# Kernel tuning notes

Measured on AMD Instinct MI355X. Metric: run time of the kernel, lower is better.

The kernel has to match this reference:

```python
import jax, jax.numpy as jnp
import numpy as np

D = 1024
D_PRE_HEAD = 128
H = 16
D_ROPE = D_PRE_HEAD // 2          # 64
DC_V = D_PRE_HEAD                 # 128
DC_KV = D_PRE_HEAD // 8           # 16
DC_Q = D // 4                     # 256
Q_HEAD_DIM = D_PRE_HEAD + D_ROPE  # 192
MEG_D = D_PRE_HEAD + DC_V         # 256
MAX_LEN = 8192
EPS = 1e-7


def rms_norm(x, w):
    x32 = x.astype(jnp.float32)
    var = jnp.mean(x32 * x32, axis=-1, keepdims=True)
    return w * (x32 * jax.lax.rsqrt(var + EPS)).astype(x.dtype)


def rope_cos_sin():
    inv_freq = 1.0 / (10000.0 ** (jnp.arange(0, D_ROPE, 2, dtype=jnp.float32) / D_ROPE))
    freqs = jnp.outer(jnp.arange(MAX_LEN, dtype=jnp.float32), inv_freq)
    emb = jnp.concatenate([freqs, freqs], axis=-1)  # [MAX_LEN, D_ROPE]
    return jnp.cos(emb), jnp.sin(emb)


def rope_reshape(x):
    # view(...,d//2,2).transpose(-1,-2).reshape == concat(even, odd) along last dim
    return jnp.concatenate([x[..., 0::2], x[..., 1::2]], axis=-1)


def rope_rotate(x):
    h = x.shape[-1] // 2
    return jnp.concatenate([-x[..., h:], x[..., :h]], axis=-1)


def setup_inputs() -> dict:
    key = jax.random.key(0)
    ks = jax.random.split(key, 12)
    B, SQ, SKV = 2, 2048, 2048
    s = 0.02
    return {
        "q_inputs": jax.random.normal(ks[0], (B, SQ, D), jnp.float32),
        "kv_input": jax.random.normal(ks[1], (B, SKV, D), jnp.float32),
        "q_pos_ids": jax.random.randint(ks[2], (B, SQ), 0, MAX_LEN),
        "kv_pos_ids": jax.random.randint(ks[3], (B, SKV), 0, MAX_LEN),
        # weights stored as [in, out] (torch Linear weight transposed)
        "Wq_down": jax.random.normal(ks[4], (D, DC_Q), jnp.float32) * s,
        "q_norm_w": jnp.ones((DC_Q,), jnp.float32),
        "Wq_up": jax.random.normal(ks[5], (DC_Q, H * Q_HEAD_DIM), jnp.float32) * s,
        "Wkv_down": jax.random.normal(ks[6], (D, DC_KV + D_ROPE), jnp.float32) * s,
        "kv_norm_w": jnp.ones((DC_KV,), jnp.float32),
        "Wkv_up": jax.random.normal(ks[7], (DC_KV, H * MEG_D), jnp.float32) * s,
        "Wout": jax.random.normal(ks[8], (H * DC_V, D), jnp.float32) * s,
    }


def reference(q_inputs, kv_input, q_pos_ids, kv_pos_ids,
              Wq_down, q_norm_w, Wq_up, Wkv_down, kv_norm_w, Wkv_up, Wout):
    B, SQ, _ = q_inputs.shape
    SKV = kv_input.shape[1]

    # query path: low-rank down -> RMSNorm -> up
    q = rms_norm(q_inputs @ Wq_down, q_norm_w) @ Wq_up
    q = q.reshape(B, SQ, H, Q_HEAD_DIM).transpose(0, 2, 1, 3)  # [B,H,SQ,192]
    q_nope, q_rope = q[..., :D_PRE_HEAD], q[..., D_PRE_HEAD:]

    # kv path: compressed latent + decoupled rope slice
    ckv_full = kv_input @ Wkv_down                              # [B,SKV,DC_KV+D_ROPE]
    c_kv, k_rope = ckv_full[..., :DC_KV], ckv_full[..., DC_KV:]
    c_kv = rms_norm(c_kv, kv_norm_w)
    kv = (c_kv @ Wkv_up).reshape(B, SKV, H, MEG_D).transpose(0, 2, 1, 3)
    k_nope, value = kv[..., :D_PRE_HEAD], kv[..., D_PRE_HEAD:]  # [B,H,SKV,128] each
    k_rope = k_rope[:, None, :, :]                              # [B,1,SKV,64]

    # RoPE with per-token position ids
    cos, sin = rope_cos_sin()
    q_cos, q_sin = cos[q_pos_ids][:, None], sin[q_pos_ids][:, None]   # [B,1,SQ,64]
    k_cos, k_sin = cos[kv_pos_ids][:, None], sin[kv_pos_ids][:, None]
    qr = rope_reshape(q_rope)
    kr = rope_reshape(k_rope)
    q_rope = qr * q_cos + rope_rotate(qr) * q_sin
    k_rope = kr * k_cos + rope_rotate(kr) * k_sin

    query = jnp.concatenate([q_nope, q_rope], axis=-1)                         # [B,H,SQ,192]
    key_t = jnp.concatenate([k_nope, jnp.broadcast_to(k_rope, (B, H, SKV, D_ROPE))], axis=-1)

    scale = 1.0 / jnp.sqrt(jnp.asarray(Q_HEAD_DIM, query.dtype))
    scores = jnp.einsum('bhqd,bhkd->bhqk', query, key_t) * scale
    attn = jax.nn.softmax(scores, axis=-1)
    out = jnp.einsum('bhqk,bhkd->bhqd', attn, value)                           # [B,H,SQ,128]
    out = out.transpose(0, 2, 1, 3).reshape(B, SQ, H * DC_V)
    return out @ Wout
```

## Files before the change

kernel.cpp:

```cpp
#include <hip/hip_runtime.h>

typedef unsigned short u16;
typedef unsigned int u32;
typedef u16 u16x4 __attribute__((ext_vector_type(4)));
typedef u16 u16x8 __attribute__((ext_vector_type(8)));
typedef u32 u32x4 __attribute__((ext_vector_type(4)));
typedef float f32x4 __attribute__((ext_vector_type(4)));
typedef __bf16 bf16x8 __attribute__((ext_vector_type(8)));
typedef __bf16 bf16x2 __attribute__((ext_vector_type(2)));

#define DEV static __device__ __forceinline__

DEV float bf2f(u16 u) { u32 v = ((u32)u) << 16; float f; __builtin_memcpy(&f, &v, 4); return f; }
DEV u16 f2bf(float f) { u32 v; __builtin_memcpy(&v, &f, 4); v += 0x7fffu + ((v >> 16) & 1u); return (u16)(v >> 16); }
DEV bf16x8 ld_frag(const u16* p) { u16x8 v = *(const u16x8*)p; return __builtin_bit_cast(bf16x8, v); }

#define LOG10000 9.210340372f

__global__ __launch_bounds__(256) void k_wtrans5(
    const float* __restrict__ Wqd, const float* __restrict__ Wqu, const float* __restrict__ Wkvd,
    const float* __restrict__ Wkvu, const float* __restrict__ Wo,
    u16* __restrict__ WqdT, u16* __restrict__ WquT, u16* __restrict__ WkvdT,
    u16* __restrict__ WkvuT, u16* __restrict__ WoT) {
  __shared__ float tile[32][33];
  int id = blockIdx.x;
  const float* in; u16* out; int R, C, Rp, bx, by;
  if (id < 256)       { in = Wqd;  out = WqdT;  R = 1024; C = 256;  Rp = 1024; bx = id & 7;  by = id >> 3; }
  else if (id < 1024) { id -= 256;  in = Wqu;  out = WquT;  R = 256;  C = 3072; Rp = 256;  bx = id % 96; by = id / 96; }
  else if (id < 1152) { id -= 1024; in = Wkvd; out = WkvdT; R = 1024; C = 80;   Rp = 1024; bx = id & 3;  by = id >> 2; }
  else if (id < 1280) { id -= 1152; in = Wkvu; out = WkvuT; R = 16;   C = 4096; Rp = 32;   bx = id;      by = 0; }
  else                { id -= 1280; in = Wo;   out = WoT;   R = 2048; C = 1024; Rp = 2048; bx = id & 31; by = id >> 5; }
  int c0 = bx * 32, r0 = by * 32;
  int tx = threadIdx.x & 31, ty = threadIdx.x >> 5;
#pragma unroll
  for (int p = 0; p < 4; p++) {
    int r = r0 + ty + p * 8, c = c0 + tx;
    tile[ty + p * 8][tx] = (r < R && c < C) ? in[(size_t)r * C + c] : 0.f;
  }
  __syncthreads();
#pragma unroll
  for (int p = 0; p < 4; p++)
    out[(size_t)(c0 + ty + p * 8) * Rp + r0 + tx] = f2bf(tile[tx][ty + p * 8]);
}

DEV void gemm64f_body(int m0, int n0, const float* __restrict__ A, const u16* __restrict__ Bt,
                      float* __restrict__ C, int N, int K, int tid, u16* As, u16* Bs) {
  constexpr int LSTR = 40;
  const int l = tid & 63, w = tid >> 6;
  const int wr = (w >> 1) * 32, wc = (w & 1) * 32;
  const int lr = l & 15, lk = (l >> 4) * 8;
  const int sr = tid >> 2, sc = (tid & 3) * 8;
  f32x4 acc[2][2] = {};
  const float* pa0 = A + (size_t)(m0 + sr) * K + sc;
  const u16* pb0 = Bt + (size_t)(n0 + sr) * K + sc;
  f32x4 vaa = *(const f32x4*)pa0, vab = *(const f32x4*)(pa0 + 4);
  u16x8 vb0 = *(const u16x8*)pb0;
  for (int k0 = 0; k0 < K; k0 += 32) {
    u16x8 va0 = { f2bf(vaa[0]), f2bf(vaa[1]), f2bf(vaa[2]), f2bf(vaa[3]),
                  f2bf(vab[0]), f2bf(vab[1]), f2bf(vab[2]), f2bf(vab[3]) };
    *(u16x8*)&As[sr * LSTR + sc] = va0;
    *(u16x8*)&Bs[sr * LSTR + sc] = vb0;
    __syncthreads();
    if (k0 + 32 < K) {
      vaa = *(const f32x4*)(pa0 + k0 + 32);
      vab = *(const f32x4*)(pa0 + k0 + 36);
      vb0 = *(const u16x8*)(pb0 + k0 + 32);
    }
    bf16x8 af[2], bf[2];
#pragma unroll
    for (int i = 0; i < 2; i++) af[i] = ld_frag(&As[(wr + i * 16 + lr) * LSTR + lk]);
#pragma unroll
    for (int j = 0; j < 2; j++) bf[j] = ld_frag(&Bs[(wc + j * 16 + lr) * LSTR + lk]);
#pragma unroll
    for (int i = 0; i < 2; i++)
#pragma unroll
      for (int j = 0; j < 2; j++)
        acc[i][j] = __builtin_amdgcn_mfma_f32_16x16x32_bf16(af[i], bf[j], acc[i][j], 0, 0, 0);
    __syncthreads();
  }
#pragma unroll
  for (int i = 0; i < 2; i++)
#pragma unroll
    for (int j = 0; j < 2; j++) {
      int row = m0 + wr + i * 16 + (l >> 4) * 4;
      int col = n0 + wc + j * 16 + lr;
#pragma unroll
      for (int r = 0; r < 4; r++)
        C[(size_t)(row + r) * N + col] = acc[i][j][r];
    }
}

__global__ __launch_bounds__(256) void k_downs(const float* __restrict__ q_in, const float* __restrict__ kv_in,
                                               const u16* __restrict__ WqdT, const u16* __restrict__ WkvdT,
                                               float* __restrict__ cq, float* __restrict__ ckvf) {
  __shared__ u16 As[64 * 40], Bs[64 * 40];
  int id = blockIdx.x, tid = threadIdx.x;
  if (id < 128) {
    int swzb = (id & 7) * 16 + (id >> 3);
    gemm64f_body((swzb >> 1) * 64, (swzb & 1) * 64, kv_in, WkvdT, ckvf, 128, 1024, tid, As, Bs);
  } else {
    int lin = id - 128;
    int swzb = (lin & 7) * 32 + (lin >> 3);
    gemm64f_body((swzb >> 2) * 64, (swzb & 3) * 64, q_in, WqdT, cq, 256, 1024, tid, As, Bs);
  }
}

__global__ __launch_bounds__(256) void k_norms(const float* __restrict__ ckvf, const float* __restrict__ kvnw,
                                               const int* __restrict__ kpos, u16* __restrict__ ckvn,
                                               u16* __restrict__ kropeb,
                                               const float* __restrict__ cq, const float* __restrict__ qnw,
                                               u16* __restrict__ cqn, float scale) {
  int id = blockIdx.x, tid = threadIdx.x;
  int l = tid & 63;
  if (id < 1024) {
    int row = id * 4 + (tid >> 6);
    const float* x = ckvf + (size_t)row * 128;
    float v = (l < 16) ? x[l] : 0.f;
    float ss = v * v;
    ss += __shfl_xor(ss, 1); ss += __shfl_xor(ss, 2); ss += __shfl_xor(ss, 4); ss += __shfl_xor(ss, 8);
    if (l < 16) ckvn[(size_t)row * 32 + l] = f2bf(v * rsqrtf(ss * (1.f / 16.f) + 1e-7f) * kvnw[l]);
    if (l >= 16 && l < 32) ckvn[(size_t)row * 32 + l] = 0;
    if (l < 32) {
      float invf = __expf(-(LOG10000 / 32.f) * (float)l);
      float ang = (float)kpos[row] * invf;
      float c = cosf(ang), s = sinf(ang);
      float e = x[16 + 2 * l], o = x[17 + 2 * l];
      kropeb[(size_t)row * 64 + l]      = f2bf(e * c - o * s);
      kropeb[(size_t)row * 64 + l + 32] = f2bf(o * c + e * s);
    }
  } else {
    int row = (id - 1024) * 4 + (tid >> 6);
    const float* x = cq + (size_t)row * 256;
    f32x4 v = *(const f32x4*)(x + l * 4);
    float ss = v[0] * v[0] + v[1] * v[1] + v[2] * v[2] + v[3] * v[3];
#pragma unroll
    for (int m = 1; m < 64; m <<= 1) ss += __shfl_xor(ss, m);
    float rinv = rsqrtf(ss * (1.f / 256.f) + 1e-7f) * scale;
    const f32x4 wv = *(const f32x4*)(qnw + l * 4);
    u16x4 o = { f2bf(v[0] * rinv * wv[0]), f2bf(v[1] * rinv * wv[1]),
                f2bf(v[2] * rinv * wv[2]), f2bf(v[3] * rinv * wv[3]) };
    *(u16x4*)(cqn + (size_t)row * 256 + l * 4) = o;
  }
}

template <int MODE>
DEV void gemm128_body(int m0, int n0, const u16* __restrict__ A, const u16* __restrict__ Bt,
                      u16* __restrict__ C0, u16* __restrict__ C1, int N, int K, int tid,
                      u16* As, u16* Bs) {
  constexpr int LSTR = 40;
  const int l = tid & 63, w = tid >> 6;
  const int wr = (w >> 1) * 64, wc = (w & 1) * 64;
  const int lr = l & 15, lk = (l >> 4) * 8;
  const int sr = tid >> 2, sc = (tid & 3) * 8;
  f32x4 acc[4][4] = {};
  const u16* pa0 = A + (size_t)(m0 + sr) * K + sc;
  const u16* pa1 = A + (size_t)(m0 + 64 + sr) * K + sc;
  const u16* pb0 = Bt + (size_t)(n0 + sr) * K + sc;
  const u16* pb1 = Bt + (size_t)(n0 + 64 + sr) * K + sc;
  u16x8 va0 = *(const u16x8*)pa0, va1 = *(const u16x8*)pa1;
  u16x8 vb0 = *(const u16x8*)pb0, vb1 = *(const u16x8*)pb1;
  for (int k0 = 0; k0 < K; k0 += 32) {
    *(u16x8*)&As[sr * LSTR + sc] = va0;
    *(u16x8*)&As[(64 + sr) * LSTR + sc] = va1;
    *(u16x8*)&Bs[sr * LSTR + sc] = vb0;
    *(u16x8*)&Bs[(64 + sr) * LSTR + sc] = vb1;
    __syncthreads();
    if (k0 + 32 < K) {
      va0 = *(const u16x8*)(pa0 + k0 + 32);
      va1 = *(const u16x8*)(pa1 + k0 + 32);
      vb0 = *(const u16x8*)(pb0 + k0 + 32);
      vb1 = *(const u16x8*)(pb1 + k0 + 32);
    }
    bf16x8 af[4], bf[4];
#pragma unroll
    for (int i = 0; i < 4; i++) af[i] = ld_frag(&As[(wr + i * 16 + lr) * LSTR + lk]);
#pragma unroll
    for (int j = 0; j < 4; j++) bf[j] = ld_frag(&Bs[(wc + j * 16 + lr) * LSTR + lk]);
#pragma unroll
    for (int i = 0; i < 4; i++)
#pragma unroll
      for (int j = 0; j < 4; j++)
        acc[i][j] = __builtin_amdgcn_mfma_f32_16x16x32_bf16(af[i], bf[j], acc[i][j], 0, 0, 0);
    __syncthreads();
  }
  if (MODE == 0 || (n0 & 255) < 128) {
#pragma unroll
    for (int i = 0; i < 4; i++)
#pragma unroll
      for (int j = 0; j < 4; j++) {
        int row = m0 + wr + i * 16 + (l >> 4) * 4;
        int col = n0 + wc + j * 16 + lr;
#pragma unroll
        for (int r = 0; r < 4; r++)
          C0[(size_t)(row + r) * N + col] = f2bf(acc[i][j][r]);
      }
  } else {
#pragma unroll
    for (int i = 0; i < 4; i++)
#pragma unroll
      for (int j = 0; j < 4; j++) {
        int row = m0 + wr + i * 16 + (l >> 4) * 4;
        int col = n0 + wc + j * 16 + lr;
        int bb = row >> 11, srow = row & 2047;
        int hh2 = col >> 8, d = col & 127;
        u16x4 pk = { f2bf(acc[i][j][0]), f2bf(acc[i][j][1]),
                     f2bf(acc[i][j][2]), f2bf(acc[i][j][3]) };
        *(u16x4*)&C1[((size_t)(bb * 16 + hh2) * 128 + d) * 2048 + srow] = pk;
      }
  }
}

__global__ __launch_bounds__(256) void k_ups(const u16* __restrict__ ckvn, const u16* __restrict__ WkvuT,
                                             u16* __restrict__ Ckv, u16* __restrict__ VTb,
                                             const u16* __restrict__ cqn, const u16* __restrict__ WquT,
                                             u16* __restrict__ qproj) {
  __shared__ u16 As[128 * 40], Bs[128 * 40];
  int id = blockIdx.x, tid = threadIdx.x;
  if (id < 1024) {
    int swzb = (id & 7) * 128 + (id >> 3);
    gemm128_body<1>((swzb >> 5) * 128, (swzb & 31) * 128, ckvn, WkvuT, Ckv, VTb, 4096, 32, tid, As, Bs);
  } else {
    int lin = id - 1024;
    int swzb = (lin & 7) * 96 + (lin >> 3);
    gemm128_body<0>((swzb / 24) * 128, (swzb % 24) * 128, cqn, WquT, qproj, nullptr, 3072, 256, tid, As, Bs);
  }
}

__global__ __launch_bounds__(256) void k_gemmh(const u16* __restrict__ A, const u16* __restrict__ Bt,
                                               float* __restrict__ Cv, int M, int N, int K) {
  constexpr int LSTR = 40;
  __shared__ u16 As[64 * LSTR], Bs[128 * LSTR];
  const int tid = threadIdx.x, l = tid & 63, w = tid >> 6;
  const int nwg = gridDim.x * gridDim.y;
  const int lin = blockIdx.y * gridDim.x + blockIdx.x;
  const int swzb = (lin & 7) * (nwg >> 3) + (lin >> 3);
  const int m0 = (swzb / gridDim.x) * 64, n0 = (swzb % gridDim.x) * 128;
  const int wr = (w >> 1) * 32, wc = (w & 1) * 64;
  const int lr = l & 15, lk = (l >> 4) * 8;
  const int sr = tid >> 2, sc = (tid & 3) * 8;
  f32x4 acc[2][4] = {};
  const u16* pa0 = A + (size_t)(m0 + sr) * K + sc;
  const u16* pb0 = Bt + (size_t)(n0 + sr) * K + sc;
  const u16* pb1 = Bt + (size_t)(n0 + 64 + sr) * K + sc;
  u16x8 va0 = *(const u16x8*)pa0;
  u16x8 vb0 = *(const u16x8*)pb0, vb1 = *(const u16x8*)pb1;
  for (int k0 = 0; k0 < K; k0 += 32) {
    *(u16x8*)&As[sr * LSTR + sc] = va0;
    *(u16x8*)&Bs[sr * LSTR + sc] = vb0;
    *(u16x8*)&Bs[(64 + sr) * LSTR + sc] = vb1;
    __syncthreads();
    if (k0 + 32 < K) {
      va0 = *(const u16x8*)(pa0 + k0 + 32);
      vb0 = *(const u16x8*)(pb0 + k0 + 32);
      vb1 = *(const u16x8*)(pb1 + k0 + 32);
    }
    bf16x8 af[2], bf[4];
#pragma unroll
    for (int i = 0; i < 2; i++) af[i] = ld_frag(&As[(wr + i * 16 + lr) * LSTR + lk]);
#pragma unroll
    for (int j = 0; j < 4; j++) bf[j] = ld_frag(&Bs[(wc + j * 16 + lr) * LSTR + lk]);
#pragma unroll
    for (int i = 0; i < 2; i++)
#pragma unroll
      for (int j = 0; j < 4; j++)
        acc[i][j] = __builtin_amdgcn_mfma_f32_16x16x32_bf16(af[i], bf[j], acc[i][j], 0, 0, 0);
    __syncthreads();
  }
#pragma unroll
  for (int i = 0; i < 2; i++)
#pragma unroll
    for (int j = 0; j < 4; j++) {
      int row = m0 + wr + i * 16 + (l >> 4) * 4;
      int col = n0 + wc + j * 16 + lr;
#pragma unroll
      for (int r = 0; r < 4; r++)
        Cv[(size_t)(row + r) * N + col] = acc[i][j][r];
    }
}

__global__ __launch_bounds__(256) void k_qrope(u16* __restrict__ q, const int* __restrict__ pos) {
  __shared__ float cs[32], sn[32];
  int bs = blockIdx.x, tid = threadIdx.x;
  if (tid < 32) {
    float invf = __expf(-(LOG10000 / 32.f) * (float)tid);
    float ang = (float)pos[bs] * invf;
    cs[tid] = cosf(ang); sn[tid] = sinf(ang);
  }
  __syncthreads();
  u16* base = q + (size_t)bs * 3072;
  int h0 = tid >> 5, p0 = tid & 31;
  int h1 = h0 + 8, p1 = p0;
  u16* r0p = base + h0 * 192 + 128;
  u16* r1p = base + h1 * 192 + 128;
  float e0 = bf2f(r0p[2 * p0]), o0 = bf2f(r0p[2 * p0 + 1]);
  float e1 = bf2f(r1p[2 * p1]), o1 = bf2f(r1p[2 * p1 + 1]);
  __syncthreads();
  r0p[p0]      = f2bf(e0 * cs[p0] - o0 * sn[p0]);
  r0p[p0 + 32] = f2bf(o0 * cs[p0] + e0 * sn[p0]);
  r1p[p1]      = f2bf(e1 * cs[p1] - o1 * sn[p1]);
  r1p[p1 + 32] = f2bf(o1 * cs[p1] + e1 * sn[p1]);
}

__global__ __launch_bounds__(512, 2) void k_attn(const u16* __restrict__ Qp, const u16* __restrict__ Ckv,
                                                 const u16* __restrict__ kropeb, const u16* __restrict__ VT,
                                                 u16* __restrict__ AO) {
  __shared__ u16 Ks[64 * 192];
  __shared__ u16 Vs[128 * 64];
  const int tid = threadIdx.x, l = tid & 63, w = tid >> 6;
  const int lr = l & 15, g = l >> 4, lk = g * 8;
  const int bid = blockIdx.x, bh = bid & 31, qt = bid >> 5;
  const int b = bh >> 4, hh = bh & 15;
  const int m0 = qt * 128;
  const u32 swz = (u32)(lr & 7) << 3;

  bf16x8 qa[6];
  {
    const u16* qrow = Qp + (size_t)(b * 2048 + m0 + w * 16 + lr) * 3072 + hh * 192;
#pragma unroll
    for (int kk = 0; kk < 6; kk++) qa[kk] = ld_frag(qrow + kk * 32 + lk);
  }

  const u16* kptr[3]; int kstep[3]; u32 klds[3];
#pragma unroll
  for (int p = 0; p < 3; p++) {
    int c2 = tid + p * 512;
    int r = c2 / 24, cc = c2 - r * 24;
    klds[p] = (u32)(r * 192 + cc * 8) ^ ((u32)(r & 7) << 3);
    if (cc < 16) { kptr[p] = Ckv + ((size_t)(b * 2048 + r)) * 4096 + hh * 256 + cc * 8; kstep[p] = 64 * 4096; }
    else         { kptr[p] = kropeb + ((size_t)(b * 2048 + r)) * 64 + (cc - 16) * 8;    kstep[p] = 64 * 64; }
  }
  const u16* vptr[2]; u32 vlds[2];
#pragma unroll
  for (int p = 0; p < 2; p++) {
    int c2 = tid + p * 512;
    int d = c2 >> 3, cc = c2 & 7;
    vlds[p] = (u32)(d * 64 + cc * 8) ^ ((u32)(d & 7) << 3);
    vptr[p] = VT + ((size_t)bh * 128 + d) * 2048 + cc * 8;
  }
  u16x8 kreg[3], vreg[2];
#pragma unroll
  for (int p = 0; p < 3; p++) { kreg[p] = *(const u16x8*)kptr[p]; kptr[p] += kstep[p]; }
#pragma unroll
  for (int p = 0; p < 2; p++) { vreg[p] = *(const u16x8*)vptr[p]; vptr[p] += 64; }

  f32x4 oacc[8] = {};
  float lsum = 0.f;
  const int srcA = lr + ((l & 16) << 1);
  const int srcB = srcA + 16;
  const bool hi = (l & 32) != 0;

  for (int t = 0; t < 32; t++) {
#pragma unroll
    for (int p = 0; p < 3; p++) *(u16x8*)&Ks[klds[p]] = kreg[p];
#pragma unroll
    for (int p = 0; p < 2; p++) *(u16x8*)&Vs[vlds[p]] = vreg[p];
    __syncthreads();
    if (t + 1 < 32) {
#pragma unroll
      for (int p = 0; p < 3; p++) { kreg[p] = *(const u16x8*)kptr[p]; kptr[p] += kstep[p]; }
#pragma unroll
      for (int p = 0; p < 2; p++) { vreg[p] = *(const u16x8*)vptr[p]; vptr[p] += 64; }
    }
    f32x4 sacc[4] = {};
    __builtin_amdgcn_s_setprio(1);
#pragma unroll
    for (int n = 0; n < 4; n++)
#pragma unroll
      for (int kk = 0; kk < 6; kk++)
        sacc[n] = __builtin_amdgcn_mfma_f32_16x16x32_bf16(
            ld_frag(&Ks[(u32)((n * 16 + lr) * 192 + kk * 32 + lk) ^ swz]), qa[kk], sacc[n], 0, 0, 0);
    __builtin_amdgcn_s_setprio(0);
    u32 pw[4][2];
#pragma unroll
    for (int n = 0; n < 4; n++) {
      float p0 = __expf(sacc[n][0]), p1 = __expf(sacc[n][1]),
            p2 = __expf(sacc[n][2]), p3 = __expf(sacc[n][3]);
      lsum += (p0 + p1) + (p2 + p3);
      bf16x2 a01 = { (__bf16)p0, (__bf16)p1 };
      bf16x2 a23 = { (__bf16)p2, (__bf16)p3 };
      pw[n][0] = __builtin_bit_cast(u32, a01);
      pw[n][1] = __builtin_bit_cast(u32, a23);
    }
    u32 pa32[2][4];
#pragma unroll
    for (int kk2 = 0; kk2 < 2; kk2++) {
      u32 t0a = __shfl(pw[2 * kk2][0], srcA), t1a = __shfl(pw[2 * kk2 + 1][0], srcA);
      u32 t0b = __shfl(pw[2 * kk2][1], srcA), t1b = __shfl(pw[2 * kk2 + 1][1], srcA);
      u32 t0c = __shfl(pw[2 * kk2][0], srcB), t1c = __shfl(pw[2 * kk2 + 1][0], srcB);
      u32 t0d = __shfl(pw[2 * kk2][1], srcB), t1d = __shfl(pw[2 * kk2 + 1][1], srcB);
      pa32[kk2][0] = hi ? t1a : t0a;
      pa32[kk2][1] = hi ? t1b : t0b;
      pa32[kk2][2] = hi ? t1c : t0c;
      pa32[kk2][3] = hi ? t1d : t0d;
    }
    __builtin_amdgcn_s_setprio(1);
#pragma unroll
    for (int kk2 = 0; kk2 < 2; kk2++) {
      u32x4 pv = { pa32[kk2][0], pa32[kk2][1], pa32[kk2][2], pa32[kk2][3] };
      bf16x8 paf = __builtin_bit_cast(bf16x8, pv);
#pragma unroll
      for (int n2 = 0; n2 < 8; n2++)
        oacc[n2] = __builtin_amdgcn_mfma_f32_16x16x32_bf16(
            paf, ld_frag(&Vs[(u32)((n2 * 16 + lr) * 64 + kk2 * 32 + lk) ^ swz]), oacc[n2], 0, 0, 0);
    }
    __builtin_amdgcn_s_setprio(0);
    __syncthreads();
  }
  float s = lsum;
  s += __shfl_xor(s, 16);
  s += __shfl_xor(s, 32);
  float rl = 1.f / s;
  float rlv[4];
#pragma unroll
  for (int r = 0; r < 4; r++) rlv[r] = __shfl(rl, g * 4 + r);
#pragma unroll
  for (int n2 = 0; n2 < 8; n2++)
#pragma unroll
    for (int r = 0; r < 4; r++) {
      int row = m0 + w * 16 + g * 4 + r;
      AO[((size_t)(b * 2048 + row) * 16 + hh) * 128 + n2 * 16 + lr] = f2bf(oacc[n2][r] * rlv[r]);
    }
}

extern "C" void kernel_launch(void* const* d_in, const int* in_sizes, int n_in,
                              void* d_out, int out_size, void* d_ws, size_t ws_size,
                              hipStream_t stream) {
  const float* q_in  = (const float*)d_in[0];
  const float* kv_in = (const float*)d_in[1];
  const int*   qpos  = (const int*)d_in[2];
  const int*   kpos  = (const int*)d_in[3];
  const float* Wqd   = (const float*)d_in[4];
  const float* qnw   = (const float*)d_in[5];
  const float* Wqu   = (const float*)d_in[6];
  const float* Wkvd  = (const float*)d_in[7];
  const float* kvnw  = (const float*)d_in[8];
  const float* Wkvu  = (const float*)d_in[9];
  const float* Wo    = (const float*)d_in[10];
  float* out = (float*)d_out;
  char* ws = (char*)d_ws;
  size_t off = 0;
  auto alloc = [&](size_t bytes) -> void* {
    void* p = ws + off; off += (bytes + 255) & ~(size_t)255; return p;
  };
  u16*   WqdT   = (u16*)alloc(256ull * 1024 * 2);
  u16*   WquT   = (u16*)alloc(3072ull * 256 * 2);
  u16*   WkvdT  = (u16*)alloc(128ull * 1024 * 2);
  u16*   WkvuT  = (u16*)alloc(4096ull * 32 * 2);
  u16*   WoT    = (u16*)alloc(1024ull * 2048 * 2);
  float* ckvf   = (float*)alloc(4096ull * 128 * 4);
  u16*   ckvn   = (u16*)alloc(4096ull * 32 * 2);
  u16*   kropeb = (u16*)alloc(4096ull * 64 * 2);
  u16*   Ckv    = (u16*)alloc(4096ull * 4096 * 2);
  u16*   VTb    = (u16*)alloc(32ull * 128 * 2048 * 2);
  float* cq     = (float*)alloc(4096ull * 256 * 4);
  u16*   cqn    = (u16*)alloc(4096ull * 256 * 2);
  u16*   qproj  = (u16*)alloc(4096ull * 3072 * 2);
  u16*   AOb    = (u16*)alloc(4096ull * 2048 * 2);
  (void)in_sizes; (void)n_in; (void)out_size; (void)ws_size;

  k_wtrans5<<<3328, 256, 0, stream>>>(Wqd, Wqu, Wkvd, Wkvu, Wo, WqdT, WquT, WkvdT, WkvuT, WoT);
  k_downs<<<384, 256, 0, stream>>>(q_in, kv_in, WqdT, WkvdT, cq, ckvf);
  k_norms<<<2048, 256, 0, stream>>>(ckvf, kvnw, kpos, ckvn, kropeb, cq, qnw, cqn, 0.07216878364870322f);
  k_ups<<<1792, 256, 0, stream>>>(ckvn, WkvuT, Ckv, VTb, cqn, WquT, qproj);
  k_qrope<<<4096, 256, 0, stream>>>(qproj, qpos);
  k_attn<<<512, 512, 0, stream>>>(qproj, Ckv, kropeb, VTb, AOb);
  k_gemmh<<<dim3(8, 64), 256, 0, stream>>>(AOb, WoT, out, 4096, 1024, 2048);
}
```

Before: 213.1 us.

## Fuse query RoPE into attention and double the KV tile to 128

Removes the standalone query-RoPE kernel. The rotation is now applied inside the attention kernel while the Q fragments are loaded into registers, with cos/sin computed per lane. This saves a kernel launch and a full read-modify-write pass over the query projection. The KV tile per iteration also grows from 64 to 128 keys, halving the loop trips and barriers. The cost is 80KB of LDS per block, which makes two blocks per CU a tight fit, plus more live registers for staging and probabilities, so spills are possible.

```diff
diff --git a/kernel.cpp b/kernel.cpp
--- a/kernel.cpp
+++ b/kernel.cpp
@@ -278,34 +278,11 @@
     }
 }
 
-__global__ __launch_bounds__(256) void k_qrope(u16* __restrict__ q, const int* __restrict__ pos) {
-  __shared__ float cs[32], sn[32];
-  int bs = blockIdx.x, tid = threadIdx.x;
-  if (tid < 32) {
-    float invf = __expf(-(LOG10000 / 32.f) * (float)tid);
-    float ang = (float)pos[bs] * invf;
-    cs[tid] = cosf(ang); sn[tid] = sinf(ang);
-  }
-  __syncthreads();
-  u16* base = q + (size_t)bs * 3072;
-  int h0 = tid >> 5, p0 = tid & 31;
-  int h1 = h0 + 8, p1 = p0;
-  u16* r0p = base + h0 * 192 + 128;
-  u16* r1p = base + h1 * 192 + 128;
-  float e0 = bf2f(r0p[2 * p0]), o0 = bf2f(r0p[2 * p0 + 1]);
-  float e1 = bf2f(r1p[2 * p1]), o1 = bf2f(r1p[2 * p1 + 1]);
-  __syncthreads();
-  r0p[p0]      = f2bf(e0 * cs[p0] - o0 * sn[p0]);
-  r0p[p0 + 32] = f2bf(o0 * cs[p0] + e0 * sn[p0]);
-  r1p[p1]      = f2bf(e1 * cs[p1] - o1 * sn[p1]);
-  r1p[p1 + 32] = f2bf(o1 * cs[p1] + e1 * sn[p1]);
-}
-
 __global__ __launch_bounds__(512, 2) void k_attn(const u16* __restrict__ Qp, const u16* __restrict__ Ckv,
                                                  const u16* __restrict__ kropeb, const u16* __restrict__ VT,
-                                                 u16* __restrict__ AO) {
-  __shared__ u16 Ks[64 * 192];
-  __shared__ u16 Vs[128 * 64];
+                                                 const int* __restrict__ qpos, u16* __restrict__ AO) {
+  __shared__ u16 Ks[128 * 192];
+  __shared__ u16 Vs[128 * 128];
   const int tid = threadIdx.x, l = tid & 63, w = tid >> 6;
   const int lr = l & 15, g = l >> 4, lk = g * 8;
   const int bid = blockIdx.x, bh = bid & 31, qt = bid >> 5;
@@ -315,33 +292,50 @@
 
   bf16x8 qa[6];
   {
-    const u16* qrow = Qp + (size_t)(b * 2048 + m0 + w * 16 + lr) * 3072 + hh * 192;
-#pragma unroll
-    for (int kk = 0; kk < 6; kk++) qa[kk] = ld_frag(qrow + kk * 32 + lk);
-  }
-
-  const u16* kptr[3]; int kstep[3]; u32 klds[3];
-#pragma unroll
-  for (int p = 0; p < 3; p++) {
+    const int rowi = b * 2048 + m0 + w * 16 + lr;
+    const u16* qrow = Qp + (size_t)rowi * 3072 + hh * 192;
+#pragma unroll
+    for (int kk = 0; kk < 4; kk++) qa[kk] = ld_frag(qrow + kk * 32 + lk);
+    u16x8 e0 = *(const u16x8*)(qrow + 128 + 16 * g);
+    u16x8 e1 = *(const u16x8*)(qrow + 136 + 16 * g);
+    float fpos = (float)qpos[rowi];
+    u16x8 r4, r5;
+#pragma unroll
+    for (int i = 0; i < 8; i++) {
+      float invf = __expf(-(LOG10000 / 32.f) * (float)(8 * g + i));
+      float ang = fpos * invf;
+      float c = cosf(ang), s = sinf(ang);
+      float ev = bf2f(i < 4 ? e0[2 * i] : e1[2 * i - 8]);
+      float od = bf2f(i < 4 ? e0[2 * i + 1] : e1[2 * i - 7]);
+      r4[i] = f2bf(ev * c - od * s);
+      r5[i] = f2bf(od * c + ev * s);
+    }
+    qa[4] = __builtin_bit_cast(bf16x8, r4);
+    qa[5] = __builtin_bit_cast(bf16x8, r5);
+  }
+
+  const u16* kptr[6]; int kstep[6]; u32 klds[6];
+#pragma unroll
+  for (int p = 0; p < 6; p++) {
     int c2 = tid + p * 512;
     int r = c2 / 24, cc = c2 - r * 24;
     klds[p] = (u32)(r * 192 + cc * 8) ^ ((u32)(r & 7) << 3);
-    if (cc < 16) { kptr[p] = Ckv + ((size_t)(b * 2048 + r)) * 4096 + hh * 256 + cc * 8; kstep[p] = 64 * 4096; }
-    else         { kptr[p] = kropeb + ((size_t)(b * 2048 + r)) * 64 + (cc - 16) * 8;    kstep[p] = 64 * 64; }
-  }
-  const u16* vptr[2]; u32 vlds[2];
-#pragma unroll
-  for (int p = 0; p < 2; p++) {
+    if (cc < 16) { kptr[p] = Ckv + ((size_t)(b * 2048 + r)) * 4096 + hh * 256 + cc * 8; kstep[p] = 128 * 4096; }
+    else         { kptr[p] = kropeb + ((size_t)(b * 2048 + r)) * 64 + (cc - 16) * 8;    kstep[p] = 128 * 64; }
+  }
+  const u16* vptr[4]; u32 vlds[4];
+#pragma unroll
+  for (int p = 0; p < 4; p++) {
     int c2 = tid + p * 512;
-    int d = c2 >> 3, cc = c2 & 7;
-    vlds[p] = (u32)(d * 64 + cc * 8) ^ ((u32)(d & 7) << 3);
+    int d = c2 >> 4, cc = c2 & 15;
+    vlds[p] = (u32)(d * 128 + cc * 8) ^ ((u32)(d & 7) << 3);
     vptr[p] = VT + ((size_t)bh * 128 + d) * 2048 + cc * 8;
   }
-  u16x8 kreg[3], vreg[2];
-#pragma unroll
-  for (int p = 0; p < 3; p++) { kreg[p] = *(const u16x8*)kptr[p]; kptr[p] += kstep[p]; }
-#pragma unroll
-  for (int p = 0; p < 2; p++) { vreg[p] = *(const u16x8*)vptr[p]; vptr[p] += 64; }
+  u16x8 kreg[6], vreg[4];
+#pragma unroll
+  for (int p = 0; p < 6; p++) { kreg[p] = *(const u16x8*)kptr[p]; kptr[p] += kstep[p]; }
+#pragma unroll
+  for (int p = 0; p < 4; p++) { vreg[p] = *(const u16x8*)vptr[p]; vptr[p] += 128; }
 
   f32x4 oacc[8] = {};
   float lsum = 0.f;
@@ -349,59 +343,74 @@
   const int srcB = srcA + 16;
   const bool hi = (l & 32) != 0;
 
-  for (int t = 0; t < 32; t++) {
-#pragma unroll
-    for (int p = 0; p < 3; p++) *(u16x8*)&Ks[klds[p]] = kreg[p];
-#pragma unroll
-    for (int p = 0; p < 2; p++) *(u16x8*)&Vs[vlds[p]] = vreg[p];
-    __syncthreads();
-    if (t + 1 < 32) {
-#pragma unroll
-      for (int p = 0; p < 3; p++) { kreg[p] = *(const u16x8*)kptr[p]; kptr[p] += kstep[p]; }
-#pragma unroll
-      for (int p = 0; p < 2; p++) { vreg[p] = *(const u16x8*)vptr[p]; vptr[p] += 64; }
-    }
-    f32x4 sacc[4] = {};
+  for (int t = 0; t < 16; t++) {
+#pragma unroll
+    for (int p = 0; p < 6; p++) *(u16x8*)&Ks[klds[p]] = kreg[p];
+#pragma unroll
+    for (int p = 0; p < 4; p++) *(u16x8*)&Vs[vlds[p]] = vreg[p];
+    __syncthreads();
+    if (t + 1 < 16) {
+#pragma unroll
+      for (int p = 0; p < 6; p++) { kreg[p] = *(const u16x8*)kptr[p]; kptr[p] += kstep[p]; }
+#pragma unroll
+      for (int p = 0; p < 4; p++) { vreg[p] = *(const u16x8*)vptr[p]; vptr[p] += 128; }
+    }
+    u32 pw[8][2];
+    {
+      f32x4 sacc[4] = {};
+      __builtin_amdgcn_s_setprio(1);
+#pragma unroll
+      for (int n = 0; n < 4; n++)
+#pragma unroll
+        for (int kk = 0; kk < 6; kk++)
+          sacc[n] = __builtin_amdgcn_mfma_f32_16x16x32_bf16(
+              ld_frag(&Ks[(u32)((n * 16 + lr) * 192 + kk * 32 + lk) ^ swz]), qa[kk], sacc[n], 0, 0, 0);
+      __builtin_amdgcn_s_setprio(0);
+#pragma unroll
+      for (int n = 0; n < 4; n++) {
+        float p0 = __expf(sacc[n][0]), p1 = __expf(sacc[n][1]),
+              p2 = __expf(sacc[n][2]), p3 = __expf(sacc[n][3]);
+        lsum += (p0 + p1) + (p2 + p3);
+        bf16x2 a01 = { (__bf16)p0, (__bf16)p1 };
+        bf16x2 a23 = { (__bf16)p2, (__bf16)p3 };
+        pw[n][0] = __builtin_bit_cast(u32, a01);
+        pw[n][1] = __builtin_bit_cast(u32, a23);
+      }
+    }
+    {
+      f32x4 sacc[4] = {};
+      __builtin_amdgcn_s_setprio(1);
+#pragma unroll
+      for (int n = 0; n < 4; n++)
+#pragma unroll
+        for (int kk = 0; kk < 6; kk++)
+          sacc[n] = __builtin_amdgcn_mfma_f32_16x16x32_bf16(
+              ld_frag(&Ks[(u32)(((n + 4) * 16 + lr) * 192 + kk * 32 + lk) ^ swz]), qa[kk], sacc[n], 0, 0, 0);
+      __builtin_amdgcn_s_setprio(0);
+#pragma unroll
+      for (int n = 0; n < 4; n++) {
+        float p0 = __expf(sacc[n][0]), p1 = __expf(sacc[n][1]),
+              p2 = __expf(sacc[n][2]), p3 = __expf(sacc[n][3]);
+        lsum += (p0 + p1) + (p2 + p3);
+        bf16x2 a01 = { (__bf16)p0, (__bf16)p1 };
+        bf16x2 a23 = { (__bf16)p2, (__bf16)p3 };
+        pw[n + 4][0] = __builtin_bit_cast(u32, a01);
+        pw[n + 4][1] = __builtin_bit_cast(u32, a23);
+      }
+    }
     __builtin_amdgcn_s_setprio(1);
 #pragma unroll
-    for (int n = 0; n < 4; n++)
-#pragma unroll
-      for (int kk = 0; kk < 6; kk++)
-        sacc[n] = __builtin_amdgcn_mfma_f32_16x16x32_bf16(
-            ld_frag(&Ks[(u32)((n * 16 + lr) * 192 + kk * 32 + lk) ^ swz]), qa[kk], sacc[n], 0, 0, 0);
-    __builtin_amdgcn_s_setprio(0);
-    u32 pw[4][2];
-#pragma unroll
-    for (int n = 0; n < 4; n++) {
-      float p0 = __expf(sacc[n][0]), p1 = __expf(sacc[n][1]),
-            p2 = __expf(sacc[n][2]), p3 = __expf(sacc[n][3]);
-      lsum += (p0 + p1) + (p2 + p3);
-      bf16x2 a01 = { (__bf16)p0, (__bf16)p1 };
-      bf16x2 a23 = { (__bf16)p2, (__bf16)p3 };
-      pw[n][0] = __builtin_bit_cast(u32, a01);
-      pw[n][1] = __builtin_bit_cast(u32, a23);
-    }
-    u32 pa32[2][4];
-#pragma unroll
-    for (int kk2 = 0; kk2 < 2; kk2++) {
+    for (int kk2 = 0; kk2 < 4; kk2++) {
       u32 t0a = __shfl(pw[2 * kk2][0], srcA), t1a = __shfl(pw[2 * kk2 + 1][0], srcA);
       u32 t0b = __shfl(pw[2 * kk2][1], srcA), t1b = __shfl(pw[2 * kk2 + 1][1], srcA);
       u32 t0c = __shfl(pw[2 * kk2][0], srcB), t1c = __shfl(pw[2 * kk2 + 1][0], srcB);
       u32 t0d = __shfl(pw[2 * kk2][1], srcB), t1d = __shfl(pw[2 * kk2 + 1][1], srcB);
-      pa32[kk2][0] = hi ? t1a : t0a;
-      pa32[kk2][1] = hi ? t1b : t0b;
-      pa32[kk2][2] = hi ? t1c : t0c;
-      pa32[kk2][3] = hi ? t1d : t0d;
-    }
-    __builtin_amdgcn_s_setprio(1);
-#pragma unroll
-    for (int kk2 = 0; kk2 < 2; kk2++) {
-      u32x4 pv = { pa32[kk2][0], pa32[kk2][1], pa32[kk2][2], pa32[kk2][3] };
+      u32x4 pv = { hi ? t1a : t0a, hi ? t1b : t0b, hi ? t1c : t0c, hi ? t1d : t0d };
       bf16x8 paf = __builtin_bit_cast(bf16x8, pv);
 #pragma unroll
       for (int n2 = 0; n2 < 8; n2++)
         oacc[n2] = __builtin_amdgcn_mfma_f32_16x16x32_bf16(
-            paf, ld_frag(&Vs[(u32)((n2 * 16 + lr) * 64 + kk2 * 32 + lk) ^ swz]), oacc[n2], 0, 0, 0);
+            paf, ld_frag(&Vs[(u32)((n2 * 16 + lr) * 128 + kk2 * 32 + lk) ^ swz]), oacc[n2], 0, 0, 0);
     }
     __builtin_amdgcn_s_setprio(0);
     __syncthreads();
@@ -462,7 +471,6 @@
   k_downs<<<384, 256, 0, stream>>>(q_in, kv_in, WqdT, WkvdT, cq, ckvf);
   k_norms<<<2048, 256, 0, stream>>>(ckvf, kvnw, kpos, ckvn, kropeb, cq, qnw, cqn, 0.07216878364870322f);
   k_ups<<<1792, 256, 0, stream>>>(ckvn, WkvuT, Ckv, VTb, cqn, WquT, qproj);
-  k_qrope<<<4096, 256, 0, stream>>>(qproj, qpos);
-  k_attn<<<512, 512, 0, stream>>>(qproj, Ckv, kropeb, VTb, AOb);
+  k_attn<<<512, 512, 0, stream>>>(qproj, Ckv, kropeb, VTb, qpos, AOb);
   k_gemmh<<<dim3(8, 64), 256, 0, stream>>>(AOb, WoT, out, 4096, 1024, 2048);
 }
```

Result: slower. 230.1 us (+7.9%).
